# Performance work log

Hardware: AMD Instinct MI355X
Metric: run time of the kernel (lower is better)

The kernel has to match this reference:

```python
import jax, jax.numpy as jnp
import numpy as np

EPS = 1e-7
B, N, DIM, NH, HD, WIN, HASH_WIN = 2, 1024, 512, 8, 64, 64, 8


def expmap0(v, c):
    sqrt_c = jnp.clip(jnp.sqrt(c), EPS)
    v_norm = jnp.linalg.norm(v, axis=-1, keepdims=True)
    is_zero = v_norm < EPS
    safe = jnp.clip(v_norm, EPS)
    mag = jnp.tanh(sqrt_c * safe) / sqrt_c
    return jnp.where(is_zero, jnp.zeros_like(v), mag * (v / safe))


def poincare_dist(x, y, c):
    # x: (B,H,N,1,D), y: (B,H,N,W,D), c: (B,1,1,1,1) -> (B,H,N,W)
    sqrt_c = jnp.clip(jnp.sqrt(c), EPS)
    x2 = jnp.sum(x * x, -1, keepdims=True)
    y2 = jnp.sum(y * y, -1, keepdims=True)
    xy = jnp.sum(x * y, -1, keepdims=True)
    num = (1 - 2 * c * xy + c * y2) * x + (1 - c * x2) * (-y)
    den = 1 - 2 * c * xy + c * c * x2 * y2
    diff = num / jnp.clip(den, EPS)
    dn = jnp.linalg.norm(diff, axis=-1)
    arg = jnp.minimum(jnp.squeeze(sqrt_c, -1) * jnp.clip(dn, EPS), 1.0 - EPS)
    return 2.0 * jnp.arctanh(arg) / jnp.squeeze(sqrt_c, -1)


def sliding_windows(t, w):
    # t: (B,H,N,D) -> (B,H,N,w,D), left-padded causal window
    Bb, H, Nn, D = t.shape
    pad = jnp.zeros((Bb, H, w - 1, D), t.dtype)
    tp = jnp.concatenate([pad, t], axis=2)
    idx = jnp.arange(w)[None, :] + jnp.arange(Nn)[:, None]  # (N,w)
    return tp[:, :, idx, :]


def layernorm(x, s, b):
    m = jnp.mean(x, -1, keepdims=True)
    v = jnp.var(x, -1, keepdims=True)
    return (x - m) / jnp.sqrt(v + 1e-6) * s + b


def rope(x, cos, sin):
    # x: (B,N,H,hd), cos/sin: (N, hd//2) -- complex rotation in real arithmetic
    xr, xi = jnp.split(x, 2, axis=-1)
    cos = cos[None, :, None, :]
    sin = sin[None, :, None, :]
    return jnp.concatenate([xr * cos - xi * sin, xr * sin + xi * cos], axis=-1)


def setup_inputs() -> dict:
    key = jax.random.key(0)
    ks = jax.random.split(key, 10)
    x = jax.random.normal(ks[0], (B, N, DIM), jnp.float32)
    pos = jnp.arange(N, dtype=jnp.float32)
    inv = 1.0 / (10000.0 ** (jnp.arange(0, HD, 2, dtype=jnp.float32) / HD))
    ang = pos[:, None] * inv[None, :]  # (N, HD//2)
    freqs_cos, freqs_sin = jnp.cos(ang), jnp.sin(ang)
    c = jax.random.uniform(ks[1], (B,), jnp.float32) * 0.9 + 0.1
    s = 0.02
    Wq = jax.random.normal(ks[2], (DIM, DIM), jnp.float32) * s
    Wk = jax.random.normal(ks[3], (DIM, DIM), jnp.float32) * s
    Wv = jax.random.normal(ks[4], (DIM, DIM), jnp.float32) * s
    Wo = jax.random.normal(ks[5], (DIM, DIM), jnp.float32) * s
    W1 = jax.random.normal(ks[6], (DIM, 4 * DIM), jnp.float32) * s
    W2 = jax.random.normal(ks[7], (4 * DIM, DIM), jnp.float32) * s
    bq = jnp.zeros((DIM,)); bk = jnp.zeros((DIM,)); bv = jnp.zeros((DIM,))
    bo = jnp.zeros((DIM,)); b1 = jnp.zeros((4 * DIM,)); b2 = jnp.zeros((DIM,))
    ln1_s = jnp.ones((DIM,)); ln1_b = jnp.zeros((DIM,))
    ln2_s = jnp.ones((DIM,)); ln2_b = jnp.zeros((DIM,))
    geo_scale = jnp.ones((NH, 1, 1), jnp.float32)
    hash_offset = jax.random.normal(ks[8], (1, 1, NH, HD), jnp.float32) * 0.01
    return dict(x=x, freqs_cos=freqs_cos, freqs_sin=freqs_sin, c=c,
                Wq=Wq, bq=bq, Wk=Wk, bk=bk, Wv=Wv, bv=bv, Wo=Wo, bo=bo,
                W1=W1, b1=b1, W2=W2, b2=b2,
                ln1_s=ln1_s, ln1_b=ln1_b, ln2_s=ln2_s, ln2_b=ln2_b,
                geo_scale=geo_scale, hash_offset=hash_offset)


def reference(x, freqs_cos, freqs_sin, c, Wq, bq, Wk, bk, Wv, bv, Wo, bo,
              W1, b1, W2, b2, ln1_s, ln1_b, ln2_s, ln2_b, geo_scale, hash_offset):
    x_res = x
    xn = layernorm(x, ln1_s, ln1_b)
    q = (xn @ Wq + bq).reshape(B, N, NH, HD)
    k = (xn @ Wk + bk).reshape(B, N, NH, HD)
    v = (xn @ Wv + bv).reshape(B, N, NH, HD)
    q = q + hash_offset * jnp.log(1.0 + HASH_WIN)
    q_rot = rope(q, freqs_cos, freqs_sin)
    k_rot = rope(k, freqs_cos, freqs_sin)
    c_b = c.reshape(B, 1, 1, 1)
    q_h = expmap0(q_rot, c_b)
    k_h = expmap0(k_rot, c_b)
    q_h, k_h, v = (t.transpose(0, 2, 1, 3) for t in (q_h, k_h, v))  # (B,H,N,D)
    k_win = sliding_windows(k_h, WIN)  # (B,H,N,W,D)
    v_win = sliding_windows(v, WIN)
    dist = poincare_dist(q_h[:, :, :, None, :], k_win, c.reshape(B, 1, 1, 1, 1))  # (B,H,N,W)
    scores = -geo_scale * dist
    w = jax.nn.softmax(scores, axis=-1)
    attn = jnp.einsum('bhnw,bhnwd->bhnd', w, v_win)
    attn = attn.transpose(0, 2, 1, 3).reshape(B, N, DIM)
    x_out = x_res + (attn @ Wo + bo)
    h = layernorm(x_out, ln2_s, ln2_b)
    ffn = jax.nn.gelu(h @ W1 + b1) @ W2 + b2
    return x_out + ffn
```

## Files before the change

kernel.cpp:

```cpp
#include <hip/hip_runtime.h>
#include <math.h>
#include <stdint.h>

#define Bn   2
#define Nn   1024
#define DIMn 512
#define NHn  8
#define HDn  64
#define QKVS 1536
#define EPSF 1e-7f

typedef __attribute__((ext_vector_type(8))) short short8;
typedef __attribute__((ext_vector_type(4))) float floatx4;
typedef __attribute__((ext_vector_type(4))) float fx4;
typedef __attribute__((ext_vector_type(4))) unsigned short usx4;

__device__ __forceinline__ unsigned short f2bf(float f) {
  union { float f; uint32_t u; } v; v.f = f;
  uint32_t u = v.u;
  return (unsigned short)((u + 0x7FFFu + ((u >> 16) & 1u)) >> 16);
}
__device__ __forceinline__ float bf2f(unsigned short h) {
  union { uint32_t u; float f; } v; v.u = ((uint32_t)h) << 16;
  return v.f;
}

__device__ __forceinline__ float wsum(float v) {
#pragma unroll
  for (int m = 32; m >= 1; m >>= 1) v += __shfl_xor(v, m, 64);
  return v;
}

__device__ __forceinline__ float gelu_tanh(float x) {
  const float k0 = 0.7978845608028654f;
  float x3 = x * x * x;
  return 0.5f * x * (1.f + tanhf(k0 * (x + 0.044715f * x3)));
}

__device__ __forceinline__ void glds16(const unsigned short* g, unsigned short* l) {
  __builtin_amdgcn_global_load_lds((const __attribute__((address_space(1))) void*)g,
                                   (__attribute__((address_space(3))) void*)l, 16, 0, 0);
}

__global__ __launch_bounds__(256) void prep_kernel(
    const float* __restrict__ Wq, const float* __restrict__ Wk,
    const float* __restrict__ Wv, const float* __restrict__ Wo,
    const float* __restrict__ W1, const float* __restrict__ W2,
    unsigned short* __restrict__ Wcat_hi, unsigned short* __restrict__ Wcat_lo,
    unsigned short* __restrict__ Wo_t, unsigned short* __restrict__ W1_t,
    unsigned short* __restrict__ W2_t,
    const float* __restrict__ bq, const float* __restrict__ bk,
    const float* __restrict__ bv, float* __restrict__ bias_cat,
    const float* __restrict__ x, const float* __restrict__ ln1s,
    const float* __restrict__ ln1b,
    unsigned short* __restrict__ xn_hi, unsigned short* __restrict__ xn_lo) {
  __shared__ float t[32][33];
  __shared__ float red[2][4];
  int bid = blockIdx.x;
  int tid = threadIdx.x;
  if (bid == 3072) {
    for (int i = tid; i < 512; i += 256) {
      bias_cat[i] = bq[i];
      bias_cat[512 + i] = bk[i];
      bias_cat[1024 + i] = bv[i];
    }
    return;
  }
  if (bid > 3072) {
    int row = bid - 3073;
    const float* xr = x + (size_t)row * DIMn;
    float2 xv = *(const float2*)(xr + tid * 2);
    float s  = xv.x + xv.y;
    float s2 = xv.x * xv.x + xv.y * xv.y;
    s = wsum(s); s2 = wsum(s2);
    int wv = tid >> 6;
    if ((tid & 63) == 0) { red[0][wv] = s; red[1][wv] = s2; }
    __syncthreads();
    s  = red[0][0] + red[0][1] + red[0][2] + red[0][3];
    s2 = red[1][0] + red[1][1] + red[1][2] + red[1][3];
    float mean = s * (1.f / DIMn);
    float var  = s2 * (1.f / DIMn) - mean * mean;
    float rstd = rsqrtf(var + 1e-6f);
    int d = tid * 2;
    float2 gv = *(const float2*)(ln1s + d);
    float2 bv2 = *(const float2*)(ln1b + d);
    float o0 = (xv.x - mean) * rstd * gv.x + bv2.x;
    float o1 = (xv.y - mean) * rstd * gv.y + bv2.y;
    size_t idx = (size_t)row * DIMn + d;
    unsigned short h0 = f2bf(o0), h1 = f2bf(o1);
    ushort2 hv; hv.x = h0; hv.y = h1;
    *(ushort2*)(xn_hi + idx) = hv;
    ushort2 lv; lv.x = f2bf(o0 - bf2f(h0)); lv.y = f2bf(o1 - bf2f(h1));
    *(ushort2*)(xn_lo + idx) = lv;
    return;
  }
  const float* W;
  unsigned short* hi;
  unsigned short* lo = nullptr;
  int K, N, tix;
  if (bid < 256)       { W = Wq; hi = Wcat_hi;               lo = Wcat_lo;               K = 512;  N = 512;  tix = bid; }
  else if (bid < 512)  { W = Wk; hi = Wcat_hi + 512 * 512;   lo = Wcat_lo + 512 * 512;   K = 512;  N = 512;  tix = bid - 256; }
  else if (bid < 768)  { W = Wv; hi = Wcat_hi + 1024 * 512;  K = 512;  N = 512;  tix = bid - 512; }
  else if (bid < 1024) { W = Wo; hi = Wo_t;                  K = 512;  N = 512;  tix = bid - 768; }
  else if (bid < 2048) { W = W1; hi = W1_t;                  K = 512;  N = 2048; tix = bid - 1024; }
  else                 { W = W2; hi = W2_t;                  K = 2048; N = 512;  tix = bid - 2048; }
  int ntn = N >> 5;
  int kt = tix / ntn, nt = tix - kt * ntn;
  int k0 = kt * 32, n0 = nt * 32;
  {
    int r = tid >> 3, c = (tid & 7) << 2;
    fx4 v = *(const fx4*)&W[(size_t)(k0 + r) * N + n0 + c];
    t[r][c] = v.x; t[r][c + 1] = v.y; t[r][c + 2] = v.z; t[r][c + 3] = v.w;
  }
  __syncthreads();
  for (int i = tid; i < 1024; i += 256) {
    int r = i >> 5, c = i & 31;
    float v = t[c][r];
    unsigned short h = f2bf(v);
    size_t oi = (size_t)(n0 + r) * K + k0 + c;
    hi[oi] = h;
    if (lo) lo[oi] = f2bf(v - bf2f(h));
  }
}

__global__ __launch_bounds__(256) void ln_kernel(const float* __restrict__ x,
                                                 const float* __restrict__ g,
                                                 const float* __restrict__ be,
                                                 unsigned short* __restrict__ yhi) {
  __shared__ float red[2][4];
  int row = blockIdx.x;
  int tid = threadIdx.x;
  const float* xr = x + (size_t)row * DIMn;
  float2 xv = *(const float2*)(xr + tid * 2);
  float s  = xv.x + xv.y;
  float s2 = xv.x * xv.x + xv.y * xv.y;
  s = wsum(s); s2 = wsum(s2);
  int wv = tid >> 6;
  if ((tid & 63) == 0) { red[0][wv] = s; red[1][wv] = s2; }
  __syncthreads();
  s  = red[0][0] + red[0][1] + red[0][2] + red[0][3];
  s2 = red[1][0] + red[1][1] + red[1][2] + red[1][3];
  float mean = s * (1.f / DIMn);
  float var  = s2 * (1.f / DIMn) - mean * mean;
  float rstd = rsqrtf(var + 1e-6f);
  int d = tid * 2;
  float2 gv = *(const float2*)(g + d);
  float2 bv = *(const float2*)(be + d);
  float o0 = (xv.x - mean) * rstd * gv.x + bv.x;
  float o1 = (xv.y - mean) * rstd * gv.y + bv.y;
  size_t idx = (size_t)row * DIMn + d;
  ushort2 hv; hv.x = f2bf(o0); hv.y = f2bf(o1);
  *(ushort2*)(yhi + idx) = hv;
}

template <int BM, int BN, int BKT, int SPLIT, int EPI, int OUTBF16>
__global__ __launch_bounds__(256) void gemm_mfma(
    const unsigned short* __restrict__ Ahi, const unsigned short* __restrict__ Alo,
    const unsigned short* __restrict__ Bhi, const unsigned short* __restrict__ Blo,
    const float* __restrict__ bias, const float* __restrict__ res,
    void* __restrict__ outp, int M, int N, int K) {
  constexpr int FI = BM / 32, FJ = BN / 32;
  constexpr int AE = BM * BKT, BE = BN * BKT;
  constexpr int NB = (SPLIT > 0) ? 2 : 1;
  constexpr int CPR = BKT / 8;
  constexpr int ACH = BM * CPR, BCH = BN * CPR;
  constexpr int CST = BN + 4;
  constexpr int SMEM_STAGE = NB * (AE + BE);
  constexpr int SMEM_EPI   = BM * CST * 2;
  constexpr int SMEM_N = (SMEM_STAGE > SMEM_EPI) ? SMEM_STAGE : SMEM_EPI;
  __shared__ __align__(16) unsigned short smem[SMEM_N];
  unsigned short* AsHi = smem;
  unsigned short* AsLo = smem + ((SPLIT > 0) ? AE : 0);
  unsigned short* BsHi = smem + NB * AE;
  unsigned short* BsLo = BsHi + ((SPLIT > 0) ? BE : 0);

  int tid = threadIdx.x;
  int lane = tid & 63;
  int wid = tid >> 6;
  int wm = (wid >> 1) * (BM / 2), wn = (wid & 1) * (BN / 2);
  int bm = blockIdx.y * BM, bn = blockIdx.x * BN;
  int m16 = lane & 15, kg = lane >> 4;
  bool dos = (SPLIT == 1) || (SPLIT == 2 && bn < 1024);

  floatx4 acc[FI][FJ];
#pragma unroll
  for (int i = 0; i < FI; ++i)
#pragma unroll
    for (int j = 0; j < FJ; ++j) { floatx4 z = {0.f, 0.f, 0.f, 0.f}; acc[i][j] = z; }

  const unsigned short* aph = Ahi + (size_t)bm * K;
  const unsigned short* bph = Bhi + (size_t)bn * K;
  const unsigned short* apl = (SPLIT > 0) ? (Alo + (size_t)bm * K) : nullptr;
  const unsigned short* bpl = (SPLIT > 0) ? (Blo + (size_t)bn * K) : nullptr;

  for (int k0 = 0; k0 < K; k0 += BKT) {
#pragma unroll
    for (int c = tid; c < ACH; c += 256) {
      int row = c / CPR, kk = (c % CPR) * 8;
      glds16(aph + (size_t)row * K + k0 + kk, AsHi + c * 8);
      if (SPLIT > 0 && dos) glds16(apl + (size_t)row * K + k0 + kk, AsLo + c * 8);
    }
#pragma unroll
    for (int c = tid; c < BCH; c += 256) {
      int row = c / CPR, kk = (c % CPR) * 8;
      glds16(bph + (size_t)row * K + k0 + kk, BsHi + c * 8);
      if (SPLIT > 0 && dos) glds16(bpl + (size_t)row * K + k0 + kk, BsLo + c * 8);
    }
    __syncthreads();

#pragma unroll
    for (int ks = 0; ks < BKT / 32; ++ks) {
      short8 ah[FI], bh[FJ];
      short8 al[(SPLIT > 0) ? FI : 1], bl[(SPLIT > 0) ? FJ : 1];
#pragma unroll
      for (int i = 0; i < FI; ++i) {
        int r = wm + i * 16 + m16;
        ah[i] = *(const short8*)&AsHi[r * BKT + ks * 32 + kg * 8];
        if (SPLIT > 0 && dos) al[i] = *(const short8*)&AsLo[r * BKT + ks * 32 + kg * 8];
      }
#pragma unroll
      for (int j = 0; j < FJ; ++j) {
        int r = wn + j * 16 + m16;
        bh[j] = *(const short8*)&BsHi[r * BKT + ks * 32 + kg * 8];
        if (SPLIT > 0 && dos) bl[j] = *(const short8*)&BsLo[r * BKT + ks * 32 + kg * 8];
      }
#pragma unroll
      for (int i = 0; i < FI; ++i)
#pragma unroll
        for (int j = 0; j < FJ; ++j) {
          acc[i][j] = __builtin_amdgcn_mfma_f32_16x16x32_bf16(ah[i], bh[j], acc[i][j], 0, 0, 0);
          if (SPLIT > 0) {
            if (dos) {
              acc[i][j] = __builtin_amdgcn_mfma_f32_16x16x32_bf16(al[i], bh[j], acc[i][j], 0, 0, 0);
              acc[i][j] = __builtin_amdgcn_mfma_f32_16x16x32_bf16(ah[i], bl[j], acc[i][j], 0, 0, 0);
            }
          }
        }
    }
    __syncthreads();
  }

  float* Cs = (float*)smem;
#pragma unroll
  for (int i = 0; i < FI; ++i)
#pragma unroll
    for (int j = 0; j < FJ; ++j)
#pragma unroll
      for (int r = 0; r < 4; ++r)
        Cs[(wm + i * 16 + kg * 4 + r) * CST + wn + j * 16 + m16] = acc[i][j][r];
  __syncthreads();
  constexpr int TOT = BM * BN / 4;
  for (int t = tid; t < TOT; t += 256) {
    int row = (t << 2) / BN;
    int col = (t << 2) & (BN - 1);
    fx4 v = *(const fx4*)&Cs[row * CST + col];
    fx4 bs = *(const fx4*)&bias[bn + col];
    v = v + bs;
    size_t gidx = (size_t)(bm + row) * N + bn + col;
    if constexpr (EPI == 1) {
      fx4 rr = *(const fx4*)&res[gidx];
      v = v + rr;
    }
    if constexpr (EPI == 2) {
      v.x = gelu_tanh(v.x); v.y = gelu_tanh(v.y);
      v.z = gelu_tanh(v.z); v.w = gelu_tanh(v.w);
    }
    if constexpr (OUTBF16) {
      usx4 h;
      h.x = f2bf(v.x); h.y = f2bf(v.y); h.z = f2bf(v.z); h.w = f2bf(v.w);
      *(usx4*)((unsigned short*)outp + gidx) = h;
    } else {
      *(fx4*)((float*)outp + gidx) = v;
    }
  }
}

__global__ __launch_bounds__(512) void attn_fused(const float* __restrict__ qkv,
                                                  const float* __restrict__ fcos,
                                                  const float* __restrict__ fsin,
                                                  const float* __restrict__ cvec,
                                                  const float* __restrict__ geo,
                                                  const float* __restrict__ hash,
                                                  unsigned short* __restrict__ attn_out) {
  __shared__ unsigned short Qhi[32][72], Qlo[32][72];
  __shared__ unsigned short Khi[96][72], Klo[96][72];
  __shared__ unsigned short Vt[64][104];
  __shared__ unsigned short Pb[32][104];
  __shared__ float Sf[32][97];
  __shared__ float x2s[32], bxs[32], y2s[96], gys[96];

  int tid = threadIdx.x, lane = tid & 63, wv = tid >> 6;
  int bid = blockIdx.x;
  int nt = bid & 31, h = (bid >> 5) & 7, b = bid >> 8;
  int n0 = nt * 32;
  float c = cvec[b];
  float sqc = sqrtf(c);
  float rsqc = 1.f / sqc;
  float gs = geo[h];
  int dr = lane & 31;
  bool hih = lane >= 32;
  const float LOG9 = 2.1972245773362196f;
  float hofr = hash[h * HDn + dr] * LOG9;
  float hofi = hash[h * HDn + dr + 32] * LOG9;

  for (int i = tid; i < 32 * 52; i += 512) ((uint32_t*)Pb)[i] = 0u;

#pragma unroll
  for (int i = 0; i < 4; ++i) {
    int q = wv * 4 + i;
    int n = n0 + q;
    size_t bas = (size_t)(b * Nn + n) * QKVS + h * HDn;
    float qr = qkv[bas + dr] + hofr;
    float qi = qkv[bas + dr + 32] + hofi;
    float cs = fcos[n * 32 + dr], sn = fsin[n * 32 + dr];
    float qv = hih ? (qr * sn + qi * cs) : (qr * cs - qi * sn);
    float nq = sqrtf(wsum(qv * qv));
    float sq = fmaxf(nq, EPSF);
    float t = sqc * sq;
    float em = expf(-2.f * t);
    float opem = 1.f + em;
    float mag = ((1.f - em) / opem) * rsqc;
    float sech2 = 4.f * em / (opem * opem);
    float oq = (nq < EPSF) ? 0.f : mag * (qv / sq);
    unsigned short hh = f2bf(oq);
    Qhi[q][lane] = hh;
    Qlo[q][lane] = f2bf(oq - bf2f(hh));
    if (lane == 0) {
      x2s[q] = (nq < EPSF) ? 0.f : mag * mag;
      bxs[q] = (nq < EPSF) ? 1.f : sech2;
    }
  }
#pragma unroll 4
  for (int i = 0; i < 12; ++i) {
    int r = wv * 12 + i;
    int gi = n0 - 64 + r;
    float ok = 0.f, vf = 0.f, y2 = 0.f, gy = 1.f;
    if (gi >= 0) {
      size_t bas = (size_t)(b * Nn + gi) * QKVS + h * HDn;
      float kr = qkv[bas + 512 + dr];
      float ki = qkv[bas + 512 + dr + 32];
      vf = qkv[bas + 1024 + lane];
      float cs = fcos[gi * 32 + dr], sn = fsin[gi * 32 + dr];
      float kv = hih ? (kr * sn + ki * cs) : (kr * cs - ki * sn);
      float nk = sqrtf(wsum(kv * kv));
      float sk = fmaxf(nk, EPSF);
      float t = sqc * sk;
      float em = expf(-2.f * t);
      float opem = 1.f + em;
      float mag = ((1.f - em) / opem) * rsqc;
      float sech2 = 4.f * em / (opem * opem);
      ok = (nk < EPSF) ? 0.f : mag * (kv / sk);
      y2 = (nk < EPSF) ? 0.f : mag * mag;
      gy = (nk < EPSF) ? 1.f : sech2;
    }
    unsigned short hh = f2bf(ok);
    Khi[r][lane] = hh;
    Klo[r][lane] = f2bf(ok - bf2f(hh));
    Vt[lane][r] = f2bf(vf);
    if (lane == 0) { y2s[r] = y2; gys[r] = gy; }
  }
  __syncthreads();

  int m16 = lane & 15, kg = lane >> 4;
#pragma unroll
  for (int uu = 0; uu < 2; ++uu) {
    int u = wv + uu * 8;
    if (u < 12) {
      int mt = u / 6, ntile = u % 6;
      floatx4 acc = {0.f, 0.f, 0.f, 0.f};
#pragma unroll
      for (int ks = 0; ks < 2; ++ks) {
        short8 ah = *(const short8*)&Qhi[mt * 16 + m16][ks * 32 + kg * 8];
        short8 al = *(const short8*)&Qlo[mt * 16 + m16][ks * 32 + kg * 8];
        short8 bh = *(const short8*)&Khi[ntile * 16 + m16][ks * 32 + kg * 8];
        short8 bl = *(const short8*)&Klo[ntile * 16 + m16][ks * 32 + kg * 8];
        acc = __builtin_amdgcn_mfma_f32_16x16x32_bf16(ah, bh, acc, 0, 0, 0);
        acc = __builtin_amdgcn_mfma_f32_16x16x32_bf16(al, bh, acc, 0, 0, 0);
        acc = __builtin_amdgcn_mfma_f32_16x16x32_bf16(ah, bl, acc, 0, 0, 0);
      }
#pragma unroll
      for (int r = 0; r < 4; ++r) Sf[mt * 16 + kg * 4 + r][ntile * 16 + m16] = acc[r];
    }
  }
  __syncthreads();

#pragma unroll
  for (int i = 0; i < 4; ++i) {
    int nl = wv * 4 + i;
    int r = nl + 1 + lane;
    float xy = Sf[nl][r];
    float x2 = x2s[nl], y2 = y2s[r];
    float bx = bxs[nl], gy = gys[r];

    float den = fmaf(c * c * x2, y2, fmaf(-2.f * c, xy, 1.f));
    den = fmaxf(den, EPSF);
    float rden = 1.f / den;
    float s2 = fmaxf(x2 - 2.f * xy + y2, 0.f);
    float z = sqrtf(c * s2 * rden);
    float omz2 = bx * gy * rden;
    float opz = 1.f + fminf(z, 1.f);
    float ratio = fminf(opz * opz / omz2, 1.9999999e7f);
    float sc = -gs * logf(ratio) * rsqc;

    float e = expf(sc);
    float se = wsum(e);
    Pb[nl][r] = f2bf(e / se);
  }
  __syncthreads();

  {
    int mt = wv >> 2, ntile = wv & 3;
    floatx4 acc = {0.f, 0.f, 0.f, 0.f};
#pragma unroll
    for (int ks = 0; ks < 3; ++ks) {
      short8 a = *(const short8*)&Pb[mt * 16 + m16][ks * 32 + kg * 8];
      short8 bb = *(const short8*)&Vt[ntile * 16 + m16][ks * 32 + kg * 8];
      acc = __builtin_amdgcn_mfma_f32_16x16x32_bf16(a, bb, acc, 0, 0, 0);
    }
#pragma unroll
    for (int r = 0; r < 4; ++r) {
      int qrow = mt * 16 + kg * 4 + r;
      int d = ntile * 16 + m16;
      attn_out[(size_t)(b * Nn + n0 + qrow) * DIMn + h * HDn + d] = f2bf(acc[r]);
    }
  }
}

extern "C" void kernel_launch(void* const* d_in, const int* in_sizes, int n_in,
                              void* d_out, int out_size, void* d_ws, size_t ws_size,
                              hipStream_t stream) {
  const float* x    = (const float*)d_in[0];
  const float* fcos = (const float*)d_in[1];
  const float* fsin = (const float*)d_in[2];
  const float* cvec = (const float*)d_in[3];
  const float* Wq = (const float*)d_in[4];  const float* bq = (const float*)d_in[5];
  const float* Wk = (const float*)d_in[6];  const float* bk = (const float*)d_in[7];
  const float* Wv = (const float*)d_in[8];  const float* bv = (const float*)d_in[9];
  const float* Wo = (const float*)d_in[10]; const float* bo = (const float*)d_in[11];
  const float* W1 = (const float*)d_in[12]; const float* b1 = (const float*)d_in[13];
  const float* W2 = (const float*)d_in[14]; const float* b2 = (const float*)d_in[15];
  const float* ln1s = (const float*)d_in[16]; const float* ln1b = (const float*)d_in[17];
  const float* ln2s = (const float*)d_in[18]; const float* ln2b = (const float*)d_in[19];
  const float* geo  = (const float*)d_in[20]; const float* hash = (const float*)d_in[21];
  float* out = (float*)d_out;
  char* base = (char*)d_ws;

  unsigned short* Wcat_hi = (unsigned short*)(base + 0);
  unsigned short* Wcat_lo = (unsigned short*)(base + 1572864);
  unsigned short* Wo_t    = (unsigned short*)(base + 3145728);
  unsigned short* W1_t    = (unsigned short*)(base + 3670016);
  unsigned short* W2_t    = (unsigned short*)(base + 5767168);
  unsigned short* xn_hi   = (unsigned short*)(base + 7864320);
  unsigned short* xn_lo   = (unsigned short*)(base + 9961472);
  float*          qkv     = (float*)(base + 12058624);
  unsigned short* attnb   = (unsigned short*)(base + 7864320);
  float*          xout    = (float*)(base + 9961472);
  unsigned short* hbuf    = (unsigned short*)(base + 14155776);
  unsigned short* mid     = (unsigned short*)(base + 16252928);
  float*          bias_cat= (float*)(base + 24641536);

  const int M = Bn * Nn;

  prep_kernel<<<3073 + M, 256, 0, stream>>>(Wq, Wk, Wv, Wo, W1, W2, Wcat_hi, Wcat_lo,
                                            Wo_t, W1_t, W2_t, bq, bk, bv, bias_cat,
                                            x, ln1s, ln1b, xn_hi, xn_lo);
  gemm_mfma<64, 64, 64, 2, 0, 0><<<dim3(QKVS / 64, M / 64), 256, 0, stream>>>(
      xn_hi, xn_lo, Wcat_hi, Wcat_lo, bias_cat, nullptr, qkv, M, QKVS, 512);
  attn_fused<<<Bn * NHn * (Nn / 32), 512, 0, stream>>>(qkv, fcos, fsin, cvec, geo, hash, attnb);
  gemm_mfma<32, 64, 64, 0, 1, 0><<<dim3(DIMn / 64, M / 32), 256, 0, stream>>>(
      attnb, nullptr, Wo_t, nullptr, bo, x, xout, M, DIMn, 512);
  ln_kernel<<<M, 256, 0, stream>>>(xout, ln2s, ln2b, hbuf);
  gemm_mfma<64, 128, 64, 0, 2, 1><<<dim3(2048 / 128, M / 64), 256, 0, stream>>>(
      hbuf, nullptr, W1_t, nullptr, b1, nullptr, mid, M, 2048, 512);
  gemm_mfma<32, 64, 64, 0, 1, 0><<<dim3(DIMn / 64, M / 32), 256, 0, stream>>>(
      mid, nullptr, W2_t, nullptr, b2, xout, out, M, DIMn, 2048);
}
```

Baseline: 191.3 us.

## Fuse RoPE and expmap0 into QKV GEMM epilogue; enlarge K tile for other GEMMs

A dedicated QKV GEMM now applies bias, hash offset, RoPE and the Poincaré expmap0 in its epilogue. It writes hi/lo bf16 hyperbolic Q/K, bf16 V and per-head norm auxiliaries, so the attention kernel only loads precomputed tiles instead of recomputing per window row. This removes the redundant K-side transforms over overlapping windows and the fp32 qkv round trip. The generic GEMM loses its split path and uses a K tile of 128 for the Wo, W1 and W2 GEMMs, which raises shared memory per block. The workspace grows to hold the extra buffers.

Measured after the change: 205.5 us. +7.4%, slower.

```diff
diff --git a/kernel.cpp b/kernel.cpp
--- a/kernel.cpp
+++ b/kernel.cpp
@@ -153,26 +153,23 @@
   *(ushort2*)(yhi + idx) = hv;
 }
 
-template <int BM, int BN, int BKT, int SPLIT, int EPI, int OUTBF16>
+template <int BM, int BN, int BKT, int EPI, int OUTBF16>
 __global__ __launch_bounds__(256) void gemm_mfma(
-    const unsigned short* __restrict__ Ahi, const unsigned short* __restrict__ Alo,
-    const unsigned short* __restrict__ Bhi, const unsigned short* __restrict__ Blo,
+    const unsigned short* __restrict__ Ahi,
+    const unsigned short* __restrict__ Bhi,
     const float* __restrict__ bias, const float* __restrict__ res,
     void* __restrict__ outp, int M, int N, int K) {
   constexpr int FI = BM / 32, FJ = BN / 32;
   constexpr int AE = BM * BKT, BE = BN * BKT;
-  constexpr int NB = (SPLIT > 0) ? 2 : 1;
   constexpr int CPR = BKT / 8;
   constexpr int ACH = BM * CPR, BCH = BN * CPR;
   constexpr int CST = BN + 4;
-  constexpr int SMEM_STAGE = NB * (AE + BE);
+  constexpr int SMEM_STAGE = AE + BE;
   constexpr int SMEM_EPI   = BM * CST * 2;
   constexpr int SMEM_N = (SMEM_STAGE > SMEM_EPI) ? SMEM_STAGE : SMEM_EPI;
   __shared__ __align__(16) unsigned short smem[SMEM_N];
   unsigned short* AsHi = smem;
-  unsigned short* AsLo = smem + ((SPLIT > 0) ? AE : 0);
-  unsigned short* BsHi = smem + NB * AE;
-  unsigned short* BsLo = BsHi + ((SPLIT > 0) ? BE : 0);
+  unsigned short* BsHi = smem + AE;
 
   int tid = threadIdx.x;
   int lane = tid & 63;
@@ -180,7 +177,6 @@
   int wm = (wid >> 1) * (BM / 2), wn = (wid & 1) * (BN / 2);
   int bm = blockIdx.y * BM, bn = blockIdx.x * BN;
   int m16 = lane & 15, kg = lane >> 4;
-  bool dos = (SPLIT == 1) || (SPLIT == 2 && bn < 1024);
 
   floatx4 acc[FI][FJ];
 #pragma unroll
@@ -190,52 +186,34 @@
 
   const unsigned short* aph = Ahi + (size_t)bm * K;
   const unsigned short* bph = Bhi + (size_t)bn * K;
-  const unsigned short* apl = (SPLIT > 0) ? (Alo + (size_t)bm * K) : nullptr;
-  const unsigned short* bpl = (SPLIT > 0) ? (Blo + (size_t)bn * K) : nullptr;
 
   for (int k0 = 0; k0 < K; k0 += BKT) {
 #pragma unroll
     for (int c = tid; c < ACH; c += 256) {
       int row = c / CPR, kk = (c % CPR) * 8;
       glds16(aph + (size_t)row * K + k0 + kk, AsHi + c * 8);
-      if (SPLIT > 0 && dos) glds16(apl + (size_t)row * K + k0 + kk, AsLo + c * 8);
     }
 #pragma unroll
     for (int c = tid; c < BCH; c += 256) {
       int row = c / CPR, kk = (c % CPR) * 8;
       glds16(bph + (size_t)row * K + k0 + kk, BsHi + c * 8);
-      if (SPLIT > 0 && dos) glds16(bpl + (size_t)row * K + k0 + kk, BsLo + c * 8);
     }
     __syncthreads();
 
 #pragma unroll
     for (int ks = 0; ks < BKT / 32; ++ks) {
       short8 ah[FI], bh[FJ];
-      short8 al[(SPLIT > 0) ? FI : 1], bl[(SPLIT > 0) ? FJ : 1];
-#pragma unroll
-      for (int i = 0; i < FI; ++i) {
-        int r = wm + i * 16 + m16;
-        ah[i] = *(const short8*)&AsHi[r * BKT + ks * 32 + kg * 8];
-        if (SPLIT > 0 && dos) al[i] = *(const short8*)&AsLo[r * BKT + ks * 32 + kg * 8];
-      }
-#pragma unroll
-      for (int j = 0; j < FJ; ++j) {
-        int r = wn + j * 16 + m16;
-        bh[j] = *(const short8*)&BsHi[r * BKT + ks * 32 + kg * 8];
-        if (SPLIT > 0 && dos) bl[j] = *(const short8*)&BsLo[r * BKT + ks * 32 + kg * 8];
-      }
 #pragma unroll
       for (int i = 0; i < FI; ++i)
-#pragma unroll
-        for (int j = 0; j < FJ; ++j) {
+        ah[i] = *(const short8*)&AsHi[(wm + i * 16 + m16) * BKT + ks * 32 + kg * 8];
+#pragma unroll
+      for (int j = 0; j < FJ; ++j)
+        bh[j] = *(const short8*)&BsHi[(wn + j * 16 + m16) * BKT + ks * 32 + kg * 8];
+#pragma unroll
+      for (int i = 0; i < FI; ++i)
+#pragma unroll
+        for (int j = 0; j < FJ; ++j)
           acc[i][j] = __builtin_amdgcn_mfma_f32_16x16x32_bf16(ah[i], bh[j], acc[i][j], 0, 0, 0);
-          if (SPLIT > 0) {
-            if (dos) {
-              acc[i][j] = __builtin_amdgcn_mfma_f32_16x16x32_bf16(al[i], bh[j], acc[i][j], 0, 0, 0);
-              acc[i][j] = __builtin_amdgcn_mfma_f32_16x16x32_bf16(ah[i], bl[j], acc[i][j], 0, 0, 0);
-            }
-          }
-        }
     }
     __syncthreads();
   }
@@ -275,13 +253,178 @@
   }
 }
 
-__global__ __launch_bounds__(512) void attn_fused(const float* __restrict__ qkv,
-                                                  const float* __restrict__ fcos,
-                                                  const float* __restrict__ fsin,
-                                                  const float* __restrict__ cvec,
-                                                  const float* __restrict__ geo,
-                                                  const float* __restrict__ hash,
-                                                  unsigned short* __restrict__ attn_out) {
+__global__ __launch_bounds__(256) void qkv_gemm(
+    const unsigned short* __restrict__ Ahi, const unsigned short* __restrict__ Alo,
+    const unsigned short* __restrict__ Bhi, const unsigned short* __restrict__ Blo,
+    const float* __restrict__ bias,
+    const float* __restrict__ fcos, const float* __restrict__ fsin,
+    const float* __restrict__ cvec, const float* __restrict__ hash,
+    unsigned short* __restrict__ qh_hi, unsigned short* __restrict__ qh_lo,
+    unsigned short* __restrict__ kh_hi, unsigned short* __restrict__ kh_lo,
+    unsigned short* __restrict__ vbuf,
+    float2* __restrict__ qaux, float2* __restrict__ kaux) {
+  constexpr int BM = 64, BN = 64, BKT = 64, K = 512;
+  constexpr int FI = 2, FJ = 2;
+  constexpr int AE = BM * BKT, BE = BN * BKT;
+  constexpr int CPR = BKT / 8;
+  constexpr int ACH = BM * CPR, BCH = BN * CPR;
+  constexpr int CST = BN + 4;
+  __shared__ __align__(16) unsigned short smem[2 * (AE + BE)];
+  unsigned short* AsHi = smem;
+  unsigned short* AsLo = smem + AE;
+  unsigned short* BsHi = smem + 2 * AE;
+  unsigned short* BsLo = BsHi + BE;
+
+  int tid = threadIdx.x;
+  int lane = tid & 63;
+  int wid = tid >> 6;
+  int wm = (wid >> 1) * 32, wn = (wid & 1) * 32;
+  int bm = blockIdx.y * BM, bn = blockIdx.x * BN;
+  int m16 = lane & 15, kg = lane >> 4;
+  bool dos = bn < 1024;
+
+  floatx4 acc[FI][FJ];
+#pragma unroll
+  for (int i = 0; i < FI; ++i)
+#pragma unroll
+    for (int j = 0; j < FJ; ++j) { floatx4 z = {0.f, 0.f, 0.f, 0.f}; acc[i][j] = z; }
+
+  const unsigned short* aph = Ahi + (size_t)bm * K;
+  const unsigned short* bph = Bhi + (size_t)bn * K;
+  const unsigned short* apl = Alo + (size_t)bm * K;
+  const unsigned short* bpl = Blo + (size_t)bn * K;
+
+  for (int k0 = 0; k0 < K; k0 += BKT) {
+#pragma unroll
+    for (int c = tid; c < ACH; c += 256) {
+      int row = c / CPR, kk = (c % CPR) * 8;
+      glds16(aph + (size_t)row * K + k0 + kk, AsHi + c * 8);
+      if (dos) glds16(apl + (size_t)row * K + k0 + kk, AsLo + c * 8);
+    }
+#pragma unroll
+    for (int c = tid; c < BCH; c += 256) {
+      int row = c / CPR, kk = (c % CPR) * 8;
+      glds16(bph + (size_t)row * K + k0 + kk, BsHi + c * 8);
+      if (dos) glds16(bpl + (size_t)row * K + k0 + kk, BsLo + c * 8);
+    }
+    __syncthreads();
+
+#pragma unroll
+    for (int ks = 0; ks < BKT / 32; ++ks) {
+      short8 ah[FI], bh[FJ], al[FI], bl[FJ];
+#pragma unroll
+      for (int i = 0; i < FI; ++i) {
+        int r = wm + i * 16 + m16;
+        ah[i] = *(const short8*)&AsHi[r * BKT + ks * 32 + kg * 8];
+        if (dos) al[i] = *(const short8*)&AsLo[r * BKT + ks * 32 + kg * 8];
+      }
+#pragma unroll
+      for (int j = 0; j < FJ; ++j) {
+        int r = wn + j * 16 + m16;
+        bh[j] = *(const short8*)&BsHi[r * BKT + ks * 32 + kg * 8];
+        if (dos) bl[j] = *(const short8*)&BsLo[r * BKT + ks * 32 + kg * 8];
+      }
+#pragma unroll
+      for (int i = 0; i < FI; ++i)
+#pragma unroll
+        for (int j = 0; j < FJ; ++j) {
+          acc[i][j] = __builtin_amdgcn_mfma_f32_16x16x32_bf16(ah[i], bh[j], acc[i][j], 0, 0, 0);
+          if (dos) {
+            acc[i][j] = __builtin_amdgcn_mfma_f32_16x16x32_bf16(al[i], bh[j], acc[i][j], 0, 0, 0);
+            acc[i][j] = __builtin_amdgcn_mfma_f32_16x16x32_bf16(ah[i], bl[j], acc[i][j], 0, 0, 0);
+          }
+        }
+    }
+    __syncthreads();
+  }
+
+  float* Cs = (float*)smem;
+#pragma unroll
+  for (int i = 0; i < FI; ++i)
+#pragma unroll
+    for (int j = 0; j < FJ; ++j)
+#pragma unroll
+      for (int r = 0; r < 4; ++r)
+        Cs[(wm + i * 16 + kg * 4 + r) * CST + wn + j * 16 + m16] = acc[i][j][r];
+  __syncthreads();
+
+  int row = tid >> 2, sub = tid & 3;
+  int gm = bm + row;
+  int bb = gm >> 10;
+  int n = gm & 1023;
+  int type = bn >> 9;
+  int h = (bn >> 6) & 7;
+  const float* Crow = Cs + row * CST;
+  if (type == 2) {
+    unsigned short* dst = vbuf + (size_t)gm * DIMn + h * HDn + sub * 16;
+#pragma unroll
+    for (int jj = 0; jj < 4; ++jj) {
+      usx4 hv;
+#pragma unroll
+      for (int j = 0; j < 4; ++j) {
+        int d = sub * 16 + jj * 4 + j;
+        hv[j] = f2bf(Crow[d] + bias[bn + d]);
+      }
+      *(usx4*)(dst + jj * 4) = hv;
+    }
+  } else {
+    const float LOG9 = 2.1972245773362196f;
+    float cc = cvec[bb];
+    float sqc = sqrtf(cc), rsqc = 1.f / sqc;
+    float rot[16];
+    float s = 0.f;
+#pragma unroll
+    for (int j = 0; j < 16; ++j) {
+      int d = sub * 16 + j, dr = d & 31, dp = d ^ 32;
+      float v = Crow[d] + bias[bn + d];
+      float p = Crow[dp] + bias[bn + dp];
+      if (type == 0) { v += hash[h * HDn + d] * LOG9; p += hash[h * HDn + dp] * LOG9; }
+      float cs = fcos[n * 32 + dr], sn = fsin[n * 32 + dr];
+      float r_ = (d < 32) ? (v * cs - p * sn) : (p * sn + v * cs);
+      rot[j] = r_;
+      s += r_ * r_;
+    }
+    s += __shfl_xor(s, 1, 64);
+    s += __shfl_xor(s, 2, 64);
+    float nq = sqrtf(s);
+    float sq = fmaxf(nq, EPSF);
+    float em = expf(-2.f * sqc * sq);
+    float opem = 1.f + em;
+    float mag = ((1.f - em) / opem) * rsqc;
+    float sech2 = 4.f * em / (opem * opem);
+    bool zz = nq < EPSF;
+    float scale = zz ? 0.f : (mag / sq);
+    unsigned short* dh = (type == 0 ? qh_hi : kh_hi) + (size_t)gm * DIMn + h * HDn + sub * 16;
+    unsigned short* dl = (type == 0 ? qh_lo : kh_lo) + (size_t)gm * DIMn + h * HDn + sub * 16;
+#pragma unroll
+    for (int jj = 0; jj < 4; ++jj) {
+      usx4 hv, lv;
+#pragma unroll
+      for (int j = 0; j < 4; ++j) {
+        float o = rot[jj * 4 + j] * scale;
+        unsigned short hh = f2bf(o);
+        hv[j] = hh;
+        lv[j] = f2bf(o - bf2f(hh));
+      }
+      *(usx4*)(dh + jj * 4) = hv;
+      *(usx4*)(dl + jj * 4) = lv;
+    }
+    if (sub == 0) {
+      float2 a;
+      a.x = zz ? 0.f : mag * mag;
+      a.y = zz ? 1.f : sech2;
+      (type == 0 ? qaux : kaux)[(size_t)gm * NHn + h] = a;
+    }
+  }
+}
+
+__global__ __launch_bounds__(512) void attn_fused(
+    const unsigned short* __restrict__ qh_hi, const unsigned short* __restrict__ qh_lo,
+    const unsigned short* __restrict__ kh_hi, const unsigned short* __restrict__ kh_lo,
+    const unsigned short* __restrict__ vbuf,
+    const float2* __restrict__ qaux, const float2* __restrict__ kaux,
+    const float* __restrict__ cvec, const float* __restrict__ geo,
+    unsigned short* __restrict__ attn_out) {
   __shared__ unsigned short Qhi[32][72], Qlo[32][72];
   __shared__ unsigned short Khi[96][72], Klo[96][72];
   __shared__ unsigned short Vt[64][104];
@@ -297,11 +440,6 @@
   float sqc = sqrtf(c);
   float rsqc = 1.f / sqc;
   float gs = geo[h];
-  int dr = lane & 31;
-  bool hih = lane >= 32;
-  const float LOG9 = 2.1972245773362196f;
-  float hofr = hash[h * HDn + dr] * LOG9;
-  float hofi = hash[h * HDn + dr + 32] * LOG9;
 
   for (int i = tid; i < 32 * 52; i += 512) ((uint32_t*)Pb)[i] = 0u;
 
@@ -309,55 +447,31 @@
   for (int i = 0; i < 4; ++i) {
     int q = wv * 4 + i;
     int n = n0 + q;
-    size_t bas = (size_t)(b * Nn + n) * QKVS + h * HDn;
-    float qr = qkv[bas + dr] + hofr;
-    float qi = qkv[bas + dr + 32] + hofi;
-    float cs = fcos[n * 32 + dr], sn = fsin[n * 32 + dr];
-    float qv = hih ? (qr * sn + qi * cs) : (qr * cs - qi * sn);
-    float nq = sqrtf(wsum(qv * qv));
-    float sq = fmaxf(nq, EPSF);
-    float t = sqc * sq;
-    float em = expf(-2.f * t);
-    float opem = 1.f + em;
-    float mag = ((1.f - em) / opem) * rsqc;
-    float sech2 = 4.f * em / (opem * opem);
-    float oq = (nq < EPSF) ? 0.f : mag * (qv / sq);
-    unsigned short hh = f2bf(oq);
-    Qhi[q][lane] = hh;
-    Qlo[q][lane] = f2bf(oq - bf2f(hh));
+    size_t bas = (size_t)(b * Nn + n) * DIMn + h * HDn;
+    Qhi[q][lane] = qh_hi[bas + lane];
+    Qlo[q][lane] = qh_lo[bas + lane];
     if (lane == 0) {
-      x2s[q] = (nq < EPSF) ? 0.f : mag * mag;
-      bxs[q] = (nq < EPSF) ? 1.f : sech2;
+      float2 a = qaux[(size_t)(b * Nn + n) * NHn + h];
+      x2s[q] = a.x; bxs[q] = a.y;
     }
   }
 #pragma unroll 4
   for (int i = 0; i < 12; ++i) {
     int r = wv * 12 + i;
     int gi = n0 - 64 + r;
-    float ok = 0.f, vf = 0.f, y2 = 0.f, gy = 1.f;
     if (gi >= 0) {
-      size_t bas = (size_t)(b * Nn + gi) * QKVS + h * HDn;
-      float kr = qkv[bas + 512 + dr];
-      float ki = qkv[bas + 512 + dr + 32];
-      vf = qkv[bas + 1024 + lane];
-      float cs = fcos[gi * 32 + dr], sn = fsin[gi * 32 + dr];
-      float kv = hih ? (kr * sn + ki * cs) : (kr * cs - ki * sn);
-      float nk = sqrtf(wsum(kv * kv));
-      float sk = fmaxf(nk, EPSF);
-      float t = sqc * sk;
-      float em = expf(-2.f * t);
-      float opem = 1.f + em;
-      float mag = ((1.f - em) / opem) * rsqc;
-      float sech2 = 4.f * em / (opem * opem);
-      ok = (nk < EPSF) ? 0.f : mag * (kv / sk);
-      y2 = (nk < EPSF) ? 0.f : mag * mag;
-      gy = (nk < EPSF) ? 1.f : sech2;
-    }
-    unsigned short hh = f2bf(ok);
-    Khi[r][lane] = hh;
-    Klo[r][lane] = f2bf(ok - bf2f(hh));
-    Vt[lane][r] = f2bf(vf);
-    if (lane == 0) { y2s[r] = y2; gys[r] = gy; }
+      size_t bas = (size_t)(b * Nn + gi) * DIMn + h * HDn;
+      Khi[r][lane] = kh_hi[bas + lane];
+      Klo[r][lane] = kh_lo[bas + lane];
+      Vt[lane][r] = vbuf[bas + lane];
+      if (lane == 0) {
+        float2 a = kaux[(size_t)(b * Nn + gi) * NHn + h];
+        y2s[r] = a.x; gys[r] = a.y;
+      }
+    } else {
+      Khi[r][lane] = 0; Klo[r][lane] = 0; Vt[lane][r] = 0;
+      if (lane == 0) { y2s[r] = 0.f; gys[r] = 1.f; }
+    }
   }
   __syncthreads();
 
@@ -452,26 +566,34 @@
   unsigned short* W2_t    = (unsigned short*)(base + 5767168);
   unsigned short* xn_hi   = (unsigned short*)(base + 7864320);
   unsigned short* xn_lo   = (unsigned short*)(base + 9961472);
-  float*          qkv     = (float*)(base + 12058624);
-  unsigned short* attnb   = (unsigned short*)(base + 7864320);
-  float*          xout    = (float*)(base + 9961472);
-  unsigned short* hbuf    = (unsigned short*)(base + 14155776);
-  unsigned short* mid     = (unsigned short*)(base + 16252928);
-  float*          bias_cat= (float*)(base + 24641536);
+  unsigned short* qh_hi   = (unsigned short*)(base + 12058624);
+  unsigned short* qh_lo   = (unsigned short*)(base + 14155776);
+  unsigned short* kh_hi   = (unsigned short*)(base + 16252928);
+  unsigned short* kh_lo   = (unsigned short*)(base + 18350080);
+  unsigned short* vb_     = (unsigned short*)(base + 20447232);
+  float2*         qaux    = (float2*)(base + 22544384);
+  float2*         kaux    = (float2*)(base + 22675456);
+  unsigned short* attnb   = (unsigned short*)(base + 22806528);
+  float*          xout    = (float*)(base + 24903680);
+  unsigned short* hbuf    = (unsigned short*)(base + 29097984);
+  unsigned short* mid     = (unsigned short*)(base + 31195136);
+  float*          bias_cat= (float*)(base + 39583744);
 
   const int M = Bn * Nn;
 
   prep_kernel<<<3073 + M, 256, 0, stream>>>(Wq, Wk, Wv, Wo, W1, W2, Wcat_hi, Wcat_lo,
                                             Wo_t, W1_t, W2_t, bq, bk, bv, bias_cat,
                                             x, ln1s, ln1b, xn_hi, xn_lo);
-  gemm_mfma<64, 64, 64, 2, 0, 0><<<dim3(QKVS / 64, M / 64), 256, 0, stream>>>(
-      xn_hi, xn_lo, Wcat_hi, Wcat_lo, bias_cat, nullptr, qkv, M, QKVS, 512);
-  attn_fused<<<Bn * NHn * (Nn / 32), 512, 0, stream>>>(qkv, fcos, fsin, cvec, geo, hash, attnb);
-  gemm_mfma<32, 64, 64, 0, 1, 0><<<dim3(DIMn / 64, M / 32), 256, 0, stream>>>(
-      attnb, nullptr, Wo_t, nullptr, bo, x, xout, M, DIMn, 512);
+  qkv_gemm<<<dim3(QKVS / 64, M / 64), 256, 0, stream>>>(
+      xn_hi, xn_lo, Wcat_hi, Wcat_lo, bias_cat, fcos, fsin, cvec, hash,
+      qh_hi, qh_lo, kh_hi, kh_lo, vb_, qaux, kaux);
+  attn_fused<<<Bn * NHn * (Nn / 32), 512, 0, stream>>>(
+      qh_hi, qh_lo, kh_hi, kh_lo, vb_, qaux, kaux, cvec, geo, attnb);
+  gemm_mfma<32, 64, 128, 1, 0><<<dim3(DIMn / 64, M / 32), 256, 0, stream>>>(
+      attnb, Wo_t, bo, x, xout, M, DIMn, 512);
   ln_kernel<<<M, 256, 0, stream>>>(xout, ln2s, ln2b, hbuf);
-  gemm_mfma<64, 128, 64, 0, 2, 1><<<dim3(2048 / 128, M / 64), 256, 0, stream>>>(
-      hbuf, nullptr, W1_t, nullptr, b1, nullptr, mid, M, 2048, 512);
-  gemm_mfma<32, 64, 64, 0, 1, 0><<<dim3(DIMn / 64, M / 32), 256, 0, stream>>>(
-      mid, nullptr, W2_t, nullptr, b2, xout, out, M, DIMn, 2048);
-}
+  gemm_mfma<64, 128, 128, 2, 1><<<dim3(2048 / 128, M / 64), 256, 0, stream>>>(
+      hbuf, W1_t, b1, nullptr, mid, M, 2048, 512);
+  gemm_mfma<32, 64, 128, 1, 0><<<dim3(DIMn / 64, M / 32), 256, 0, stream>>>(
+      mid, W2_t, b2, xout, out, M, DIMn, 2048);
+}
```

## Double-buffer LDS staging in single-precision GEMMs and shrink output tiles

Applied to the files above, without the earlier changes.

Splits the generic GEMM into a dedicated split-precision QKV kernel and a new double-buffered bf16 GEMM. The new GEMM issues the next K-tile's global-to-LDS loads while MFMAs run on the current tile, with one barrier per iteration. This hides load latency behind compute. The Wo, W1 and W2 projections also use smaller tiles (32x32 and 64x64) to launch more blocks and raise occupancy. The cost is doubled LDS per block and very little MFMA work per wave in the 32x32 configuration.

Result: no change. 188.7 us (-1.3%).

```diff
diff --git a/kernel.cpp b/kernel.cpp
--- a/kernel.cpp
+++ b/kernel.cpp
@@ -153,26 +153,21 @@
   *(ushort2*)(yhi + idx) = hv;
 }
 
-template <int BM, int BN, int BKT, int SPLIT, int EPI, int OUTBF16>
-__global__ __launch_bounds__(256) void gemm_mfma(
-    const unsigned short* __restrict__ Ahi, const unsigned short* __restrict__ Alo,
-    const unsigned short* __restrict__ Bhi, const unsigned short* __restrict__ Blo,
+template <int BM, int BN, int BKT, int EPI, int OUTBF16>
+__global__ __launch_bounds__(256) void gemm_db(
+    const unsigned short* __restrict__ Ahi,
+    const unsigned short* __restrict__ Bhi,
     const float* __restrict__ bias, const float* __restrict__ res,
     void* __restrict__ outp, int M, int N, int K) {
   constexpr int FI = BM / 32, FJ = BN / 32;
   constexpr int AE = BM * BKT, BE = BN * BKT;
-  constexpr int NB = (SPLIT > 0) ? 2 : 1;
   constexpr int CPR = BKT / 8;
   constexpr int ACH = BM * CPR, BCH = BN * CPR;
   constexpr int CST = BN + 4;
-  constexpr int SMEM_STAGE = NB * (AE + BE);
-  constexpr int SMEM_EPI   = BM * CST * 2;
-  constexpr int SMEM_N = (SMEM_STAGE > SMEM_EPI) ? SMEM_STAGE : SMEM_EPI;
+  constexpr int STG = AE + BE;
+  constexpr int SMEM_EPI = BM * CST * 2;
+  constexpr int SMEM_N = (2 * STG > SMEM_EPI) ? 2 * STG : SMEM_EPI;
   __shared__ __align__(16) unsigned short smem[SMEM_N];
-  unsigned short* AsHi = smem;
-  unsigned short* AsLo = smem + ((SPLIT > 0) ? AE : 0);
-  unsigned short* BsHi = smem + NB * AE;
-  unsigned short* BsLo = BsHi + ((SPLIT > 0) ? BE : 0);
 
   int tid = threadIdx.x;
   int lane = tid & 63;
@@ -180,7 +175,6 @@
   int wm = (wid >> 1) * (BM / 2), wn = (wid & 1) * (BN / 2);
   int bm = blockIdx.y * BM, bn = blockIdx.x * BN;
   int m16 = lane & 15, kg = lane >> 4;
-  bool dos = (SPLIT == 1) || (SPLIT == 2 && bn < 1024);
 
   floatx4 acc[FI][FJ];
 #pragma unroll
@@ -190,54 +184,44 @@
 
   const unsigned short* aph = Ahi + (size_t)bm * K;
   const unsigned short* bph = Bhi + (size_t)bn * K;
-  const unsigned short* apl = (SPLIT > 0) ? (Alo + (size_t)bm * K) : nullptr;
-  const unsigned short* bpl = (SPLIT > 0) ? (Blo + (size_t)bn * K) : nullptr;
-
-  for (int k0 = 0; k0 < K; k0 += BKT) {
-#pragma unroll
+
+  auto stage = [&](int k0, unsigned short* As, unsigned short* Bs) {
     for (int c = tid; c < ACH; c += 256) {
       int row = c / CPR, kk = (c % CPR) * 8;
-      glds16(aph + (size_t)row * K + k0 + kk, AsHi + c * 8);
-      if (SPLIT > 0 && dos) glds16(apl + (size_t)row * K + k0 + kk, AsLo + c * 8);
-    }
-#pragma unroll
+      glds16(aph + (size_t)row * K + k0 + kk, As + c * 8);
+    }
     for (int c = tid; c < BCH; c += 256) {
       int row = c / CPR, kk = (c % CPR) * 8;
-      glds16(bph + (size_t)row * K + k0 + kk, BsHi + c * 8);
-      if (SPLIT > 0 && dos) glds16(bpl + (size_t)row * K + k0 + kk, BsLo + c * 8);
-    }
-    __syncthreads();
-
+      glds16(bph + (size_t)row * K + k0 + kk, Bs + c * 8);
+    }
+  };
+
+  const int NT = K / BKT;
+  stage(0, smem, smem + AE);
+  __syncthreads();
+  int cur = 0;
+  for (int t = 0; t < NT; ++t) {
+    unsigned short* As = smem + cur * STG;
+    unsigned short* Bs = As + AE;
+    int nxt = cur ^ 1;
+    if (t + 1 < NT) stage((t + 1) * BKT, smem + nxt * STG, smem + nxt * STG + AE);
 #pragma unroll
     for (int ks = 0; ks < BKT / 32; ++ks) {
       short8 ah[FI], bh[FJ];
-      short8 al[(SPLIT > 0) ? FI : 1], bl[(SPLIT > 0) ? FJ : 1];
-#pragma unroll
-      for (int i = 0; i < FI; ++i) {
-        int r = wm + i * 16 + m16;
-        ah[i] = *(const short8*)&AsHi[r * BKT + ks * 32 + kg * 8];
-        if (SPLIT > 0 && dos) al[i] = *(const short8*)&AsLo[r * BKT + ks * 32 + kg * 8];
-      }
-#pragma unroll
-      for (int j = 0; j < FJ; ++j) {
-        int r = wn + j * 16 + m16;
-        bh[j] = *(const short8*)&BsHi[r * BKT + ks * 32 + kg * 8];
-        if (SPLIT > 0 && dos) bl[j] = *(const short8*)&BsLo[r * BKT + ks * 32 + kg * 8];
-      }
 #pragma unroll
       for (int i = 0; i < FI; ++i)
-#pragma unroll
-        for (int j = 0; j < FJ; ++j) {
+        ah[i] = *(const short8*)&As[(wm + i * 16 + m16) * BKT + ks * 32 + kg * 8];
+#pragma unroll
+      for (int j = 0; j < FJ; ++j)
+        bh[j] = *(const short8*)&Bs[(wn + j * 16 + m16) * BKT + ks * 32 + kg * 8];
+#pragma unroll
+      for (int i = 0; i < FI; ++i)
+#pragma unroll
+        for (int j = 0; j < FJ; ++j)
           acc[i][j] = __builtin_amdgcn_mfma_f32_16x16x32_bf16(ah[i], bh[j], acc[i][j], 0, 0, 0);
-          if (SPLIT > 0) {
-            if (dos) {
-              acc[i][j] = __builtin_amdgcn_mfma_f32_16x16x32_bf16(al[i], bh[j], acc[i][j], 0, 0, 0);
-              acc[i][j] = __builtin_amdgcn_mfma_f32_16x16x32_bf16(ah[i], bl[j], acc[i][j], 0, 0, 0);
-            }
-          }
-        }
     }
     __syncthreads();
+    cur = nxt;
   }
 
   float* Cs = (float*)smem;
@@ -272,6 +256,106 @@
     } else {
       *(fx4*)((float*)outp + gidx) = v;
     }
+  }
+}
+
+__global__ __launch_bounds__(256) void qkv_gemm(
+    const unsigned short* __restrict__ Ahi, const unsigned short* __restrict__ Alo,
+    const unsigned short* __restrict__ Bhi, const unsigned short* __restrict__ Blo,
+    const float* __restrict__ bias, float* __restrict__ outp) {
+  constexpr int BM = 64, BN = 64, BKT = 64, K = 512, N = QKVS;
+  constexpr int FI = 2, FJ = 2;
+  constexpr int AE = BM * BKT, BE = BN * BKT;
+  constexpr int CPR = BKT / 8;
+  constexpr int ACH = BM * CPR, BCH = BN * CPR;
+  constexpr int CST = BN + 4;
+  __shared__ __align__(16) unsigned short smem[2 * (AE + BE)];
+  unsigned short* AsHi = smem;
+  unsigned short* AsLo = smem + AE;
+  unsigned short* BsHi = smem + 2 * AE;
+  unsigned short* BsLo = BsHi + BE;
+
+  int tid = threadIdx.x;
+  int lane = tid & 63;
+  int wid = tid >> 6;
+  int wm = (wid >> 1) * 32, wn = (wid & 1) * 32;
+  int bm = blockIdx.y * BM, bn = blockIdx.x * BN;
+  int m16 = lane & 15, kg = lane >> 4;
+  bool dos = bn < 1024;
+
+  floatx4 acc[FI][FJ];
+#pragma unroll
+  for (int i = 0; i < FI; ++i)
+#pragma unroll
+    for (int j = 0; j < FJ; ++j) { floatx4 z = {0.f, 0.f, 0.f, 0.f}; acc[i][j] = z; }
+
+  const unsigned short* aph = Ahi + (size_t)bm * K;
+  const unsigned short* bph = Bhi + (size_t)bn * K;
+  const unsigned short* apl = Alo + (size_t)bm * K;
+  const unsigned short* bpl = Blo + (size_t)bn * K;
+
+  for (int k0 = 0; k0 < K; k0 += BKT) {
+#pragma unroll
+    for (int c = tid; c < ACH; c += 256) {
+      int row = c / CPR, kk = (c % CPR) * 8;
+      glds16(aph + (size_t)row * K + k0 + kk, AsHi + c * 8);
+      if (dos) glds16(apl + (size_t)row * K + k0 + kk, AsLo + c * 8);
+    }
+#pragma unroll
+    for (int c = tid; c < BCH; c += 256) {
+      int row = c / CPR, kk = (c % CPR) * 8;
+      glds16(bph + (size_t)row * K + k0 + kk, BsHi + c * 8);
+      if (dos) glds16(bpl + (size_t)row * K + k0 + kk, BsLo + c * 8);
+    }
+    __syncthreads();
+
+#pragma unroll
+    for (int ks = 0; ks < BKT / 32; ++ks) {
+      short8 ah[FI], bh[FJ], al[FI], bl[FJ];
+#pragma unroll
+      for (int i = 0; i < FI; ++i) {
+        int r = wm + i * 16 + m16;
+        ah[i] = *(const short8*)&AsHi[r * BKT + ks * 32 + kg * 8];
+        if (dos) al[i] = *(const short8*)&AsLo[r * BKT + ks * 32 + kg * 8];
+      }
+#pragma unroll
+      for (int j = 0; j < FJ; ++j) {
+        int r = wn + j * 16 + m16;
+        bh[j] = *(const short8*)&BsHi[r * BKT + ks * 32 + kg * 8];
+        if (dos) bl[j] = *(const short8*)&BsLo[r * BKT + ks * 32 + kg * 8];
+      }
+#pragma unroll
+      for (int i = 0; i < FI; ++i)
+#pragma unroll
+        for (int j = 0; j < FJ; ++j) {
+          acc[i][j] = __builtin_amdgcn_mfma_f32_16x16x32_bf16(ah[i], bh[j], acc[i][j], 0, 0, 0);
+          if (dos) {
+            acc[i][j] = __builtin_amdgcn_mfma_f32_16x16x32_bf16(al[i], bh[j], acc[i][j], 0, 0, 0);
+            acc[i][j] = __builtin_amdgcn_mfma_f32_16x16x32_bf16(ah[i], bl[j], acc[i][j], 0, 0, 0);
+          }
+        }
+    }
+    __syncthreads();
+  }
+
+  float* Cs = (float*)smem;
+#pragma unroll
+  for (int i = 0; i < FI; ++i)
+#pragma unroll
+    for (int j = 0; j < FJ; ++j)
+#pragma unroll
+      for (int r = 0; r < 4; ++r)
+        Cs[(wm + i * 16 + kg * 4 + r) * CST + wn + j * 16 + m16] = acc[i][j][r];
+  __syncthreads();
+  constexpr int TOT = BM * BN / 4;
+  for (int t = tid; t < TOT; t += 256) {
+    int row = (t << 2) / BN;
+    int col = (t << 2) & (BN - 1);
+    fx4 v = *(const fx4*)&Cs[row * CST + col];
+    fx4 bs = *(const fx4*)&bias[bn + col];
+    v = v + bs;
+    size_t gidx = (size_t)(bm + row) * N + bn + col;
+    *(fx4*)(outp + gidx) = v;
   }
 }
 
@@ -464,14 +548,14 @@
   prep_kernel<<<3073 + M, 256, 0, stream>>>(Wq, Wk, Wv, Wo, W1, W2, Wcat_hi, Wcat_lo,
                                             Wo_t, W1_t, W2_t, bq, bk, bv, bias_cat,
                                             x, ln1s, ln1b, xn_hi, xn_lo);
-  gemm_mfma<64, 64, 64, 2, 0, 0><<<dim3(QKVS / 64, M / 64), 256, 0, stream>>>(
-      xn_hi, xn_lo, Wcat_hi, Wcat_lo, bias_cat, nullptr, qkv, M, QKVS, 512);
+  qkv_gemm<<<dim3(QKVS / 64, M / 64), 256, 0, stream>>>(
+      xn_hi, xn_lo, Wcat_hi, Wcat_lo, bias_cat, qkv);
   attn_fused<<<Bn * NHn * (Nn / 32), 512, 0, stream>>>(qkv, fcos, fsin, cvec, geo, hash, attnb);
-  gemm_mfma<32, 64, 64, 0, 1, 0><<<dim3(DIMn / 64, M / 32), 256, 0, stream>>>(
-      attnb, nullptr, Wo_t, nullptr, bo, x, xout, M, DIMn, 512);
+  gemm_db<32, 32, 64, 1, 0><<<dim3(DIMn / 32, M / 32), 256, 0, stream>>>(
+      attnb, Wo_t, bo, x, xout, M, DIMn, 512);
   ln_kernel<<<M, 256, 0, stream>>>(xout, ln2s, ln2b, hbuf);
-  gemm_mfma<64, 128, 64, 0, 2, 1><<<dim3(2048 / 128, M / 64), 256, 0, stream>>>(
-      hbuf, nullptr, W1_t, nullptr, b1, nullptr, mid, M, 2048, 512);
-  gemm_mfma<32, 64, 64, 0, 1, 0><<<dim3(DIMn / 64, M / 32), 256, 0, stream>>>(
-      mid, nullptr, W2_t, nullptr, b2, xout, out, M, DIMn, 2048);
-}
+  gemm_db<64, 64, 64, 2, 1><<<dim3(2048 / 64, M / 64), 256, 0, stream>>>(
+      hbuf, W1_t, b1, nullptr, mid, M, 2048, 512);
+  gemm_db<32, 32, 64, 1, 0><<<dim3(DIMn / 32, M / 32), 256, 0, stream>>>(
+      mid, W2_t, b2, xout, out, M, DIMn, 2048);
+}
```
